# Optimization experiments

Hardware: AMD Instinct MI355X
Metric: run time of the kernel (lower is better)

## Reference

```python
import jax, jax.numpy as jnp
import numpy as np

T, Bb, D, S = 1024, 2, 1024, 64
INIT_DECAY = 0.9


def setup_inputs() -> dict:
    key = jax.random.key(0)
    k1, k2, k3 = jax.random.split(key, 3)
    x = jax.random.normal(k1, (T, Bb, D), dtype=jnp.float32)
    z = jax.random.normal(k2, (T, Bb, D), dtype=jnp.float32)
    h0 = jnp.zeros((Bb, D, S), dtype=jnp.float32)
    init_logit = float(np.log(INIT_DECAY / (1.0 - INIT_DECAY)))
    decay_logits = jnp.full((D, S), init_logit, dtype=jnp.float32)
    B = 0.02 * jax.random.normal(k3, (D, S), dtype=jnp.float32)
    C = jnp.ones((S,), dtype=jnp.float32) / S
    return {"x": x, "z": z, "h0": h0, "decay_logits": decay_logits, "B": B, "C": C}


def reference(x, z, h0, decay_logits, B, C):
    # x, z: [T, Bb, D]; h0: [Bb, D, S]; decay_logits, B: [D, S]; C: [S]
    decay = jax.nn.sigmoid(decay_logits)  # [D, S]

    def step(h_prev, xz):
        x_t, z_t = xz  # [Bb, D]
        h_new = decay * h_prev + B * x_t[..., None]  # [Bb, D, S]
        out_t = jnp.einsum('bds,s->bd', h_new, C) * jax.nn.silu(z_t)
        return h_new, (out_t, h_new)

    _, (output, hs) = jax.lax.scan(step, h0, (x, z))
    h = jnp.concatenate([h0[None], hs], axis=0)  # [T+1, Bb, D, S]
    return output, h
```

## Files before the change

kernel.cpp:

```cpp
#include <hip/hip_runtime.h>


#define T_    1024
#define BB_   2
#define D_    1024
#define S_    64
#define SEG_  64
#define NSEG_ (T_ / SEG_)
#define NCH_  (BB_ * D_)
#define STRD_ (BB_ * D_)
#define CHB_  16
#define FG_   16
#define WS_NEED_ ((size_t)NCH_ * NSEG_ * S_ * 4)

typedef float f32x4 __attribute__((ext_vector_type(4)));

#define LDS_BARRIER() asm volatile("s_waitcnt lgkmcnt(0)\n\ts_barrier" ::: "memory")

#define DPP_ADD(x, ctrl, rm) \
  ((x) + __int_as_float(__builtin_amdgcn_update_dpp( \
        0, __float_as_int(x), (ctrl), (rm), 0xf, true)))

__device__ __forceinline__ float readlane_f(float v, int lane) {
    return __int_as_float(__builtin_amdgcn_readlane(__float_as_int(v), lane));
}

__device__ __forceinline__ float sigmoidf_(float v) {
    return 1.0f / (1.0f + __expf(-v));
}

__device__ __forceinline__ void nt_store4(float* p, f32x4 v) {
    __builtin_nontemporal_store(v, (f32x4*)p);
}
__device__ __forceinline__ void nt_store1(float* p, float v) {
    __builtin_nontemporal_store(v, p);
}

__global__ __launch_bounds__(256, 8) void slot_elman_pass1(
    const float* __restrict__ x, const float* __restrict__ dl,
    const float* __restrict__ Bm, float* __restrict__ ws)
{
    const int wave = blockIdx.x * (blockDim.x >> 6) + (threadIdx.x >> 6);
    const int lane = threadIdx.x & 63;
    const int bd   = wave & (NCH_ - 1);
    const int seg  = wave >> 11;
    const int d    = bd & (D_ - 1);
    const int ds   = d * S_ + lane;

    const float decay = sigmoidf_(dl[ds]);
    const float Bv    = Bm[ds];

    const float xg = x[(size_t)(seg * SEG_ + lane) * STRD_ + bd];

    float hl = 0.0f;
    #pragma unroll
    for (int i = 0; i < SEG_; ++i)
        hl = fmaf(decay, hl, Bv * readlane_f(xg, i));

    ws[(size_t)(bd * NSEG_ + seg) * S_ + lane] = hl;
}

__global__ __launch_bounds__(1024, 8) void slot_elman_pass2(
    const float* __restrict__ x, const float* __restrict__ z,
    const float* __restrict__ h0, const float* __restrict__ dl,
    const float* __restrict__ Bm, const float* __restrict__ C,
    const float* __restrict__ ws,
    float* __restrict__ out, float* __restrict__ h)
{
    __shared__ float stage[FG_ * CHB_ * S_];

    const int bid = blockIdx.x;
    const int seg = bid >> 7;
    const int g   = bid & 127;

    const int w    = threadIdx.x >> 6;
    const int lane = threadIdx.x & 63;
    const int bd   = g * CHB_ + w;
    const int d    = bd & (D_ - 1);
    const int ds   = d * S_ + lane;

    const float decay = sigmoidf_(dl[ds]);
    const float Bv    = Bm[ds];
    const float Cv    = C[lane];

    float dk = decay * decay;
    dk = dk * dk; dk = dk * dk; dk = dk * dk; dk = dk * dk;
    const float d64 = dk * dk;

    float hv = h0[(size_t)bd * S_ + lane];
    if (seg == 0)
        nt_store1(&h[(size_t)bd * S_ + lane], hv);

    const float* wp = ws + (size_t)bd * NSEG_ * S_ + lane;
    #pragma unroll
    for (int j = 0; j < NSEG_ - 1; ++j) {
        const float lj = wp[(size_t)j * S_];
        const float wgt = (j < seg) ? d64 : 1.0f;
        const float add = (j < seg) ? lj  : 0.0f;
        hv = fmaf(wgt, hv, add);
    }

    const float xgA = x[(size_t)(seg * SEG_ + lane) * STRD_ + bd];
    const float zgA = z[(size_t)(seg * SEG_ + lane) * STRD_ + bd];
    const float sgv = zgA * sigmoidf_(zgA);

    float outacc = 0.0f;

    for (int f = 0; f < SEG_ / FG_; ++f) {
        #pragma unroll
        for (int li = 0; li < FG_; ++li) {
            const int i = f * FG_ + li;
            const float xs = readlane_f(xgA, i);

            hv = fmaf(decay, hv, Bv * xs);

            stage[(li * CHB_ + w) * S_ + lane] = hv;

            float p = hv * Cv;
            p = DPP_ADD(p, 0x111, 0xf);
            p = DPP_ADD(p, 0x112, 0xf);
            p = DPP_ADD(p, 0x114, 0xf);
            p = DPP_ADD(p, 0x118, 0xf);
            p = DPP_ADD(p, 0x142, 0xa);
            p = DPP_ADD(p, 0x143, 0xc);

            const float ov = p * readlane_f(sgv, i);
            const float bc = readlane_f(ov, 63);
            outacc = (lane == i) ? bc : outacc;
        }

        LDS_BARRIER();

        {
            const int t1 = seg * SEG_ + f * FG_ + w + 1;
            const float* src = &stage[w * CHB_ * S_];
            float* dst = &h[((size_t)t1 * NCH_ + (size_t)g * CHB_) * S_];
            const int o = lane * 4;
            nt_store4(dst + o,       *(const f32x4*)(src + o));
            nt_store4(dst + o + 256, *(const f32x4*)(src + o + 256));
            nt_store4(dst + o + 512, *(const f32x4*)(src + o + 512));
            nt_store4(dst + o + 768, *(const f32x4*)(src + o + 768));
        }

        LDS_BARRIER();
    }

    stage[lane * 17 + w] = outacc;
    LDS_BARRIER();
    {
        const int tl = threadIdx.x >> 4;
        const int c  = threadIdx.x & 15;
        nt_store1(&out[(size_t)(seg * SEG_ + tl) * STRD_ + (size_t)g * CHB_ + c],
                  stage[tl * 17 + c]);
    }
}

__global__ __launch_bounds__(256, 2) void slot_elman_fallback(
    const float* __restrict__ x, const float* __restrict__ z,
    const float* __restrict__ h0, const float* __restrict__ dl,
    const float* __restrict__ Bm, const float* __restrict__ C,
    float* __restrict__ out, float* __restrict__ h)
{
    const int nb  = gridDim.x;
    const int cpx = nb >> 3;
    const int bid = blockIdx.x;
    const int swz = (bid & 7) * cpx + (bid >> 3);

    const int wave = swz * (blockDim.x >> 6) + (threadIdx.x >> 6);
    const int lane = threadIdx.x & 63;
    const int bd = wave & (NCH_ - 1);
    const int d  = bd & (D_ - 1);
    const int ds = d * S_ + lane;

    const float decay = sigmoidf_(dl[ds]);
    const float Bv    = Bm[ds];
    const float Cv    = C[lane];

    float hv = h0[(size_t)bd * S_ + lane];
    h[(size_t)bd * S_ + lane] = hv;

    const float* xg_p = x + (size_t)lane * STRD_ + bd;
    const float* zg_p = z + (size_t)lane * STRD_ + bd;
    float*       hp = h + (size_t)(NCH_ * S_) + (size_t)bd * S_ + lane;
    float*       op = out + (size_t)lane * STRD_ + bd;

    float xgA = xg_p[0];
    float zgA = zg_p[0];

    for (int blk = 0; blk < NSEG_; ++blk) {
        const int tb = blk * SEG_;
        const int tbn = (blk + 1 < NSEG_) ? (tb + SEG_) : tb;
        const float xgB = xg_p[(size_t)tbn * STRD_];
        const float zgB = zg_p[(size_t)tbn * STRD_];

        const float sgv = zgA * sigmoidf_(zgA);
        float outacc = 0.0f;

        #pragma unroll 8
        for (int i = 0; i < SEG_; ++i) {
            const float xs = readlane_f(xgA, i);
            hv = fmaf(decay, hv, Bv * xs);
            hp[(size_t)(tb + i) * (NCH_ * S_)] = hv;

            float p = hv * Cv;
            p = DPP_ADD(p, 0x111, 0xf);
            p = DPP_ADD(p, 0x112, 0xf);
            p = DPP_ADD(p, 0x114, 0xf);
            p = DPP_ADD(p, 0x118, 0xf);
            p = DPP_ADD(p, 0x142, 0xa);
            p = DPP_ADD(p, 0x143, 0xc);

            const float ov = p * readlane_f(sgv, i);
            const float bc = readlane_f(ov, 63);
            outacc = (lane == i) ? bc : outacc;
        }
        op[(size_t)tb * STRD_] = outacc;
        xgA = xgB; zgA = zgB;
    }
}

extern "C" void kernel_launch(void* const* d_in, const int* in_sizes, int n_in,
                              void* d_out, int out_size, void* d_ws, size_t ws_size,
                              hipStream_t stream) {
    const float* x  = (const float*)d_in[0];
    const float* z  = (const float*)d_in[1];
    const float* h0 = (const float*)d_in[2];
    const float* dl = (const float*)d_in[3];
    const float* Bm = (const float*)d_in[4];
    const float* C  = (const float*)d_in[5];

    float* out = (float*)d_out;
    float* h   = (float*)d_out + (size_t)T_ * BB_ * D_;

    if (ws_size >= WS_NEED_) {
        float* ws = (float*)d_ws;
        const int waves1 = NCH_ * NSEG_;
        const int grid1  = waves1 * 64 / 256;
        hipLaunchKernelGGL(slot_elman_pass1, dim3(grid1), dim3(256), 0, stream,
                           x, dl, Bm, ws);
        const int grid2  = (NCH_ / CHB_) * NSEG_;
        hipLaunchKernelGGL(slot_elman_pass2, dim3(grid2), dim3(1024), 0, stream,
                           x, z, h0, dl, Bm, C, ws, out, h);
    } else {
        const int waves = NCH_;
        const int grid  = waves * 64 / 256;
        hipLaunchKernelGGL(slot_elman_fallback, dim3(grid), dim3(256), 0, stream,
                           x, z, h0, dl, Bm, C, out, h);
    }
}
```

Before: 114.1 us.

## Compute output dot product from staged LDS tiles instead of per-step wave reductions

```diff
diff --git a/kernel.cpp b/kernel.cpp
--- a/kernel.cpp
+++ b/kernel.cpp
@@ -81,7 +81,8 @@
 
     const float decay = sigmoidf_(dl[ds]);
     const float Bv    = Bm[ds];
-    const float Cv    = C[lane];
+
+    const f32x4 cv = *(const f32x4*)&C[4 * (lane & 15)];
 
     float dk = decay * decay;
     dk = dk * dk; dk = dk * dk; dk = dk * dk; dk = dk * dk;
@@ -101,57 +102,48 @@
     }
 
     const float xgA = x[(size_t)(seg * SEG_ + lane) * STRD_ + bd];
-    const float zgA = z[(size_t)(seg * SEG_ + lane) * STRD_ + bd];
-    const float sgv = zgA * sigmoidf_(zgA);
-
-    float outacc = 0.0f;
 
     for (int f = 0; f < SEG_ / FG_; ++f) {
         #pragma unroll
         for (int li = 0; li < FG_; ++li) {
             const int i = f * FG_ + li;
             const float xs = readlane_f(xgA, i);
-
             hv = fmaf(decay, hv, Bv * xs);
-
             stage[(li * CHB_ + w) * S_ + lane] = hv;
-
-            float p = hv * Cv;
-            p = DPP_ADD(p, 0x111, 0xf);
-            p = DPP_ADD(p, 0x112, 0xf);
-            p = DPP_ADD(p, 0x114, 0xf);
-            p = DPP_ADD(p, 0x118, 0xf);
-            p = DPP_ADD(p, 0x142, 0xa);
-            p = DPP_ADD(p, 0x143, 0xc);
-
-            const float ov = p * readlane_f(sgv, i);
-            const float bc = readlane_f(ov, 63);
-            outacc = (lane == i) ? bc : outacc;
         }
 
         LDS_BARRIER();
 
         {
-            const int t1 = seg * SEG_ + f * FG_ + w + 1;
+            const int t  = seg * SEG_ + f * FG_ + w;
             const float* src = &stage[w * CHB_ * S_];
-            float* dst = &h[((size_t)t1 * NCH_ + (size_t)g * CHB_) * S_];
+            float* dst = &h[((size_t)(t + 1) * NCH_ + (size_t)g * CHB_) * S_];
             const int o = lane * 4;
-            nt_store4(dst + o,       *(const f32x4*)(src + o));
-            nt_store4(dst + o + 256, *(const f32x4*)(src + o + 256));
-            nt_store4(dst + o + 512, *(const f32x4*)(src + o + 512));
-            nt_store4(dst + o + 768, *(const f32x4*)(src + o + 768));
+
+            #pragma unroll
+            for (int b = 0; b < 4; ++b) {
+                const f32x4 v = *(const f32x4*)(src + o + b * 256);
+                nt_store4(dst + o + b * 256, v);
+
+                float pd = v.x * cv.x;
+                pd = fmaf(v.y, cv.y, pd);
+                pd = fmaf(v.z, cv.z, pd);
+                pd = fmaf(v.w, cv.w, pd);
+                pd = DPP_ADD(pd, 0x111, 0xf);
+                pd = DPP_ADD(pd, 0x112, 0xf);
+                pd = DPP_ADD(pd, 0x114, 0xf);
+                pd = DPP_ADD(pd, 0x118, 0xf);
+
+                if ((lane & 15) == 15) {
+                    const int chain = b * 4 + (lane >> 4);
+                    const size_t oi = (size_t)t * STRD_ + (size_t)g * CHB_ + chain;
+                    const float zv = z[oi];
+                    nt_store1(&out[oi], pd * (zv * sigmoidf_(zv)));
+                }
+            }
         }
 
         LDS_BARRIER();
-    }
-
-    stage[lane * 17 + w] = outacc;
-    LDS_BARRIER();
-    {
-        const int tl = threadIdx.x >> 4;
-        const int c  = threadIdx.x & 15;
-        nt_store1(&out[(size_t)(seg * SEG_ + tl) * STRD_ + (size_t)g * CHB_ + c],
-                  stage[tl * 17 + c]);
     }
 }
 
```

Result: slower. 144.4 us (+26.6%).

## Make pass2 blocks loop over four segments with prefetched inputs

Applied to the files above, without the earlier changes.

```diff
diff --git a/kernel.cpp b/kernel.cpp
--- a/kernel.cpp
+++ b/kernel.cpp
@@ -70,8 +70,8 @@
     __shared__ float stage[FG_ * CHB_ * S_];
 
     const int bid = blockIdx.x;
-    const int seg = bid >> 7;
     const int g   = bid & 127;
+    const int sr  = bid >> 7;
 
     const int w    = threadIdx.x >> 6;
     const int lane = threadIdx.x & 63;
@@ -87,71 +87,92 @@
     dk = dk * dk; dk = dk * dk; dk = dk * dk; dk = dk * dk;
     const float d64 = dk * dk;
 
-    float hv = h0[(size_t)bd * S_ + lane];
-    if (seg == 0)
-        nt_store1(&h[(size_t)bd * S_ + lane], hv);
-
-    const float* wp = ws + (size_t)bd * NSEG_ * S_ + lane;
+    const float hq = h0[(size_t)bd * S_ + lane];
+    if (sr == 0)
+        nt_store1(&h[(size_t)bd * S_ + lane], hq);
+
+    float wsreg[NSEG_ - 1];
+    {
+        const float* wp = ws + (size_t)bd * NSEG_ * S_ + lane;
+        #pragma unroll
+        for (int j = 0; j < NSEG_ - 1; ++j)
+            wsreg[j] = wp[(size_t)j * S_];
+    }
+
+    float xg = x[(size_t)(sr * SEG_ + lane) * STRD_ + bd];
+    float zg = z[(size_t)(sr * SEG_ + lane) * STRD_ + bd];
+
     #pragma unroll
-    for (int j = 0; j < NSEG_ - 1; ++j) {
-        const float lj = wp[(size_t)j * S_];
-        const float wgt = (j < seg) ? d64 : 1.0f;
-        const float add = (j < seg) ? lj  : 0.0f;
-        hv = fmaf(wgt, hv, add);
-    }
-
-    const float xgA = x[(size_t)(seg * SEG_ + lane) * STRD_ + bd];
-    const float zgA = z[(size_t)(seg * SEG_ + lane) * STRD_ + bd];
-    const float sgv = zgA * sigmoidf_(zgA);
-
-    float outacc = 0.0f;
-
-    for (int f = 0; f < SEG_ / FG_; ++f) {
+    for (int js = 0; js < 4; ++js) {
+        const int seg = 4 * js + sr;
+
+        float hv = hq;
         #pragma unroll
-        for (int li = 0; li < FG_; ++li) {
-            const int i = f * FG_ + li;
-            const float xs = readlane_f(xgA, i);
-
-            hv = fmaf(decay, hv, Bv * xs);
-
-            stage[(li * CHB_ + w) * S_ + lane] = hv;
-
-            float p = hv * Cv;
-            p = DPP_ADD(p, 0x111, 0xf);
-            p = DPP_ADD(p, 0x112, 0xf);
-            p = DPP_ADD(p, 0x114, 0xf);
-            p = DPP_ADD(p, 0x118, 0xf);
-            p = DPP_ADD(p, 0x142, 0xa);
-            p = DPP_ADD(p, 0x143, 0xc);
-
-            const float ov = p * readlane_f(sgv, i);
-            const float bc = readlane_f(ov, 63);
-            outacc = (lane == i) ? bc : outacc;
-        }
-
+        for (int j = 0; j < NSEG_ - 1; ++j) {
+            const float wgt = (j < seg) ? d64 : 1.0f;
+            const float add = (j < seg) ? wsreg[j] : 0.0f;
+            hv = fmaf(wgt, hv, add);
+        }
+
+        const float xgc = xg;
+        const float sgv = zg * sigmoidf_(zg);
+
+        if (js < 3) {
+            const int ns = seg + 4;
+            xg = x[(size_t)(ns * SEG_ + lane) * STRD_ + bd];
+            zg = z[(size_t)(ns * SEG_ + lane) * STRD_ + bd];
+        }
+
+        float outacc = 0.0f;
+
+        for (int f = 0; f < SEG_ / FG_; ++f) {
+            #pragma unroll
+            for (int li = 0; li < FG_; ++li) {
+                const int i = f * FG_ + li;
+                const float xs = readlane_f(xgc, i);
+
+                hv = fmaf(decay, hv, Bv * xs);
+
+                stage[(li * CHB_ + w) * S_ + lane] = hv;
+
+                float p = hv * Cv;
+                p = DPP_ADD(p, 0x111, 0xf);
+                p = DPP_ADD(p, 0x112, 0xf);
+                p = DPP_ADD(p, 0x114, 0xf);
+                p = DPP_ADD(p, 0x118, 0xf);
+                p = DPP_ADD(p, 0x142, 0xa);
+                p = DPP_ADD(p, 0x143, 0xc);
+
+                const float ov = p * readlane_f(sgv, i);
+                const float bc = readlane_f(ov, 63);
+                outacc = (lane == i) ? bc : outacc;
+            }
+
+            LDS_BARRIER();
+
+            {
+                const int t1 = seg * SEG_ + f * FG_ + w + 1;
+                const float* src = &stage[w * CHB_ * S_];
+                float* dst = &h[((size_t)t1 * NCH_ + (size_t)g * CHB_) * S_];
+                const int o = lane * 4;
+                nt_store4(dst + o,       *(const f32x4*)(src + o));
+                nt_store4(dst + o + 256, *(const f32x4*)(src + o + 256));
+                nt_store4(dst + o + 512, *(const f32x4*)(src + o + 512));
+                nt_store4(dst + o + 768, *(const f32x4*)(src + o + 768));
+            }
+
+            LDS_BARRIER();
+        }
+
+        stage[lane * 17 + w] = outacc;
         LDS_BARRIER();
-
         {
-            const int t1 = seg * SEG_ + f * FG_ + w + 1;
-            const float* src = &stage[w * CHB_ * S_];
-            float* dst = &h[((size_t)t1 * NCH_ + (size_t)g * CHB_) * S_];
-            const int o = lane * 4;
-            nt_store4(dst + o,       *(const f32x4*)(src + o));
-            nt_store4(dst + o + 256, *(const f32x4*)(src + o + 256));
-            nt_store4(dst + o + 512, *(const f32x4*)(src + o + 512));
-            nt_store4(dst + o + 768, *(const f32x4*)(src + o + 768));
-        }
-
+            const int tl = threadIdx.x >> 4;
+            const int c  = threadIdx.x & 15;
+            nt_store1(&out[(size_t)(seg * SEG_ + tl) * STRD_ + (size_t)g * CHB_ + c],
+                      stage[tl * 17 + c]);
+        }
         LDS_BARRIER();
-    }
-
-    stage[lane * 17 + w] = outacc;
-    LDS_BARRIER();
-    {
-        const int tl = threadIdx.x >> 4;
-        const int c  = threadIdx.x & 15;
-        nt_store1(&out[(size_t)(seg * SEG_ + tl) * STRD_ + (size_t)g * CHB_ + c],
-                  stage[tl * 17 + c]);
     }
 }
 
@@ -238,7 +259,7 @@
         const int grid1  = waves1 * 64 / 256;
         hipLaunchKernelGGL(slot_elman_pass1, dim3(grid1), dim3(256), 0, stream,
                            x, dl, Bm, ws);
-        const int grid2  = (NCH_ / CHB_) * NSEG_;
+        const int grid2  = 512;
         hipLaunchKernelGGL(slot_elman_pass2, dim3(grid2), dim3(1024), 0, stream,
                            x, z, h0, dl, Bm, C, ws, out, h);
     } else {
```

New measurement: 130.9 us. 14.8% more time.
